# Kernel optimization log

Hardware: AMD Instinct MI355X
Metric: run time of the kernel (lower is better)

The kernel has to match this reference:

```python
import jax, jax.numpy as jnp
import numpy as np

B, S, D = 4, 4096, 1024
DC = 1024  # d_chunk (defaults to d_model)
NUM_CLASSES = 4


def setup_inputs() -> dict:
    key = jax.random.key(0)
    ks = jax.random.split(key, 8)
    init = lambda k, shape: (jax.random.normal(k, shape, jnp.float32) * 0.02)
    return {
        "h": jax.random.normal(ks[0], (B, S, D), jnp.float32),
        "pseudo_labels": jax.random.randint(ks[1], (B, S), 0, NUM_CLASSES, jnp.int32),
        "Wl": init(ks[2], (D, NUM_CLASSES)), "bl": jnp.zeros((NUM_CLASSES,), jnp.float32),
        "Wq": init(ks[3], (D, DC)), "bq": jnp.zeros((DC,), jnp.float32),
        "Wk": init(ks[4], (D, DC)), "bk": jnp.zeros((DC,), jnp.float32),
        "Wv": init(ks[5], (D, D)), "bv": jnp.zeros((D,), jnp.float32),
        "Wo": init(ks[6], (D, D)), "bo": jnp.zeros((D,), jnp.float32),
    }


def _chunk_starts(labels):
    """BIOS chunking: label 0=B starts a chunk extended by following 1=I's;
    labels 1 (orphan I), 2=O, 3=S are singleton chunks. Returns bool [B,S]
    marking chunk starts. Parallel replacement for the torch while-loop."""
    def step(ext, lab):  # ext[b]: previous token can be extended by an I
        cont = (lab == 1) & ext          # this token continues prev chunk
        new_ext = (lab == 0) | cont      # B, or a continuing I, is extendable
        return new_ext, ~cont            # non-continuing token starts a chunk
    init = jnp.zeros(labels.shape[0], dtype=bool)
    _, starts_t = jax.lax.scan(step, init, labels.T)  # scan over seq axis
    return starts_t.T  # [B, S]


def reference(h, pseudo_labels, Wl, bl, Wq, bq, Wk, bk, Wv, bv, Wo, bo):
    b, s, d = h.shape
    dc = Wq.shape[1]

    logits = h @ Wl + bl                                  # [B,S,4]
    logp = jax.nn.log_softmax(logits, axis=-1)
    loss = -jnp.mean(jnp.take_along_axis(logp, pseudo_labels[..., None], axis=-1))

    pred = jnp.argmax(logits, axis=-1).astype(jnp.int32)  # [B,S]
    starts = _chunk_starts(pred)
    seg = jnp.cumsum(starts.astype(jnp.int32), axis=1) - 1  # segment id per token

    # Segment-mean pooling, padded to S possible chunks per batch element.
    seg_sum = jax.vmap(lambda x, ids: jax.ops.segment_sum(x, ids, num_segments=s))(h, seg)
    counts = jax.vmap(lambda ids: jax.ops.segment_sum(jnp.ones((s,), h.dtype), ids, num_segments=s))(seg)
    chunk_emb = seg_sum / jnp.maximum(counts, 1.0)[..., None]  # [B,S,D]
    valid = counts > 0                                         # [B,S]

    q = h @ Wq + bq              # [B,S,DC]
    k = chunk_emb @ Wk + bk      # [B,C,DC]
    v = chunk_emb @ Wv + bv      # [B,C,D]
    scale = jnp.asarray(1.0 / np.sqrt(dc), h.dtype)
    scores = jnp.einsum('bsd,bcd->bsc', q, k) * scale
    scores = jnp.where(valid[:, None, :], scores, jnp.asarray(-1e30, h.dtype))
    attn = jax.nn.softmax(scores, axis=-1)
    attended = jnp.einsum('bsc,bcd->bsd', attn, v)
    ch_out = attended @ Wo + bo
    return ch_out, loss
```

## Files before the change

kernel.cpp:

```cpp
#include <hip/hip_runtime.h>

typedef unsigned short u16;
typedef __attribute__((ext_vector_type(8))) short short8;
typedef __attribute__((ext_vector_type(8))) unsigned short ushort8;
typedef __attribute__((ext_vector_type(4))) unsigned short ushort4v;
typedef __attribute__((ext_vector_type(4))) float f32x4;

#define NB 4
#define SS 4096
#define DD 1024
#define CFENCE asm volatile("" ::: "memory")

__device__ __forceinline__ u16 f2bf(float x) {
  unsigned u = __builtin_bit_cast(unsigned, x);
  u = (u + 0x7FFFu + ((u >> 16) & 1u)) >> 16;
  return (u16)u;
}
__device__ __forceinline__ float bf2f(u16 b) {
  unsigned u = ((unsigned)b) << 16;
  return __builtin_bit_cast(float, u);
}
__device__ __forceinline__ void gload16(const void* g, void* l) {
  __builtin_amdgcn_global_load_lds((const __attribute__((address_space(1))) void*)g,
                                   (__attribute__((address_space(3))) void*)l, 16, 0, 0);
}
__device__ __forceinline__ int xcd_swz(int bid, int nwg) {
  const int x = bid & 7, idx = bid >> 3;
  const int q = nwg >> 3, r = nwg & 7;
  return (x < r ? x * (q + 1) : r * (q + 1) + (x - r) * q) + idx;
}

__global__ __launch_bounds__(256) void k_logits(
    const float* __restrict__ h, const int* __restrict__ lab,
    const float* __restrict__ Wl, const float* __restrict__ bl,
    u16* __restrict__ h16, int* __restrict__ pred, float* __restrict__ lossPart)
{
  const int t = threadIdx.x, w = t >> 6, lane = t & 63;
  const int tok = blockIdx.x * 4 + w;
  const float4* h4p = (const float4*)(h + (size_t)tok * DD);
  const float4* wl4 = (const float4*)Wl;
  float p0 = 0.f, p1 = 0.f, p2 = 0.f, p3 = 0.f;
#pragma unroll
  for (int i = 0; i < 4; ++i) {
    const int d = i * 256 + lane * 4;
    float4 hv = h4p[i * 64 + lane];
    ushort4v hb;
    hb[0] = f2bf(hv.x); hb[1] = f2bf(hv.y); hb[2] = f2bf(hv.z); hb[3] = f2bf(hv.w);
    *(ushort4v*)(h16 + (size_t)tok * DD + d) = hb;
    float4 w0 = wl4[d], w1 = wl4[d + 1], w2 = wl4[d + 2], w3 = wl4[d + 3];
    p0 += hv.x * w0.x + hv.y * w1.x + hv.z * w2.x + hv.w * w3.x;
    p1 += hv.x * w0.y + hv.y * w1.y + hv.z * w2.y + hv.w * w3.y;
    p2 += hv.x * w0.z + hv.y * w1.z + hv.z * w2.z + hv.w * w3.z;
    p3 += hv.x * w0.w + hv.y * w1.w + hv.z * w2.w + hv.w * w3.w;
  }
#pragma unroll
  for (int m = 32; m; m >>= 1) {
    p0 += __shfl_xor(p0, m); p1 += __shfl_xor(p1, m);
    p2 += __shfl_xor(p2, m); p3 += __shfl_xor(p3, m);
  }
  __shared__ float ls[4];
  if (lane == 0) {
    float l[4] = {p0 + bl[0], p1 + bl[1], p2 + bl[2], p3 + bl[3]};
    int bi = 0; float bv = l[0];
#pragma unroll
    for (int c = 1; c < 4; ++c) if (l[c] > bv) { bv = l[c]; bi = c; }
    pred[tok] = bi;
    float se = 0.f;
#pragma unroll
    for (int c = 0; c < 4; ++c) se += expf(l[c] - bv);
    float lse = bv + logf(se);
    ls[w] = lse - l[lab[tok]];
  }
  __syncthreads();
  if (t == 0) lossPart[blockIdx.x] = ls[0] + ls[1] + ls[2] + ls[3];
}

__global__ __launch_bounds__(256) void k_wconv(
    const float* __restrict__ W0, const float* __restrict__ W1,
    const float* __restrict__ W2, const float* __restrict__ W3,
    u16* __restrict__ Wt)
{
  const int gid = blockIdx.x * 256 + threadIdx.x;
  const int mat = gid >> 20;
  const int rem = gid & ((1 << 20) - 1);
  const int n = rem >> 10, k = rem & 1023;
  const float* W = (mat == 0) ? W0 : (mat == 1) ? W1 : (mat == 2) ? W2 : W3;
  Wt[((size_t)mat << 20) + (size_t)n * 1024 + k] = f2bf(W[(size_t)k * 1024 + n]);
}

__global__ __launch_bounds__(256) void k_scan(
    const int* __restrict__ pred, int* __restrict__ cstart, int* __restrict__ ccnt)
{
  const int b = blockIdx.x, t = threadIdx.x;
  const int4* p4 = (const int4*)(pred + (size_t)b * SS);
  int labv[16];
#pragma unroll
  for (int i = 0; i < 4; ++i) {
    int4 v = p4[t * 4 + i];
    labv[i * 4 + 0] = v.x; labv[i * 4 + 1] = v.y;
    labv[i * 4 + 2] = v.z; labv[i * 4 + 3] = v.w;
  }
  int A = 0, Bc = 1;
#pragma unroll
  for (int e = 0; e < 16; ++e) {
    int a = (labv[e] == 0), bb = (labv[e] == 1);
    A = a | (bb & A);
    Bc = bb & Bc;
  }
  __shared__ int sA[256], sB[256], sC[256];
  sA[t] = A; sB[t] = Bc;
  __syncthreads();
  for (int off = 1; off < 256; off <<= 1) {
    int pa = 0, pb = 1;
    if (t >= off) { pa = sA[t - off]; pb = sB[t - off]; }
    __syncthreads();
    A = A | (Bc & pa); Bc = Bc & pb;
    sA[t] = A; sB[t] = Bc;
    __syncthreads();
  }
  const int extIn = (t == 0) ? 0 : sA[t - 1];
  int ext = extIn, nst = 0;
#pragma unroll
  for (int e = 0; e < 16; ++e) {
    int cont = (labv[e] == 1) & ext;
    nst += !cont;
    ext = (labv[e] == 0) | cont;
  }
  sC[t] = nst;
  __syncthreads();
  int tot = nst;
  for (int off = 1; off < 256; off <<= 1) {
    int pc = 0;
    if (t >= off) pc = sC[t - off];
    __syncthreads();
    tot += pc;
    sC[t] = tot;
    __syncthreads();
  }
  const int base = tot - nst;
  const int total = sC[255];
  if (t == 0) { ccnt[b] = total; cstart[b * (SS + 1) + total] = SS; }
  ext = extIn; int id = base;
#pragma unroll
  for (int e = 0; e < 16; ++e) {
    int cont = (labv[e] == 1) & ext;
    if (!cont) cstart[b * (SS + 1) + id++] = t * 16 + e;
    ext = (labv[e] == 0) | cont;
  }
}

__global__ __launch_bounds__(256) void k_pool(
    const float* __restrict__ h, const int* __restrict__ cstart,
    const int* __restrict__ ccnt, u16* __restrict__ cemb)
{
  const int t = threadIdx.x, w = t >> 6, lane = t & 63;
  const int gw = blockIdx.x * 4 + w;
  const int b = gw >> 12, c = gw & (SS - 1);
  u16* out = cemb + (size_t)gw * DD + lane * 16;
  if (c >= ccnt[b]) {
    ushort8 z = {0, 0, 0, 0, 0, 0, 0, 0};
    *(ushort8*)out = z; *(ushort8*)(out + 8) = z;
    return;
  }
  const int s0 = cstart[b * (SS + 1) + c], s1 = cstart[b * (SS + 1) + c + 1];
  float acc[16] = {};
  for (int s = s0; s < s1; ++s) {
    const float4* hp = (const float4*)(h + ((size_t)b * SS + s) * DD + lane * 16);
#pragma unroll
    for (int ii = 0; ii < 4; ++ii) {
      float4 v = hp[ii];
      acc[ii * 4 + 0] += v.x; acc[ii * 4 + 1] += v.y;
      acc[ii * 4 + 2] += v.z; acc[ii * 4 + 3] += v.w;
    }
  }
  const float inv = 1.f / (float)(s1 - s0);
  ushort8 o0, o1;
#pragma unroll
  for (int e = 0; e < 8; ++e) { o0[e] = f2bf(acc[e] * inv); o1[e] = f2bf(acc[8 + e] * inv); }
  *(ushort8*)out = o0; *(ushort8*)(out + 8) = o1;
}

template <int OUTF32>
__global__ __launch_bounds__(512, 2) void gemm256(
    const u16* __restrict__ A0, const u16* __restrict__ A1,
    const u16* __restrict__ A2, const u16* __restrict__ A3,
    const u16* __restrict__ Bt, long strideB,
    void* __restrict__ C0, void* __restrict__ C1,
    void* __restrict__ C2, void* __restrict__ C3,
    const float* __restrict__ bias, float scale, int M, int N, int K)
{
  __shared__ u16 lds[65536];
  u16* ldsA = lds;
  u16* ldsB = lds + 32768;
  const int t = threadIdx.x, lane = t & 63, w = t >> 6;
  const int wr = w >> 2, wc = w & 3;
  const int z = blockIdx.z;
  const u16* A = (z == 0) ? A0 : (z == 1) ? A1 : (z == 2) ? A2 : A3;
  void* Cp    = (z == 0) ? C0 : (z == 1) ? C1 : (z == 2) ? C2 : C3;
  const u16* B = Bt + (size_t)z * strideB;
  const int bid = blockIdx.y * gridDim.x + blockIdx.x;
  const int swz = xcd_swz(bid, gridDim.x * gridDim.y);
  const int m0 = (swz / gridDim.x) * 256, n0 = (swz % gridDim.x) * 256;

  f32x4 acc[8][4];
#pragma unroll
  for (int i = 0; i < 8; ++i)
#pragma unroll
    for (int j = 0; j < 4; ++j) acc[i][j] = (f32x4){0.f, 0.f, 0.f, 0.f};

  const int trow = t >> 3;
  const u16* Ag = A + (size_t)(m0 + trow) * K + ((t & 7) ^ (trow & 7)) * 8;
  const u16* Bg = B + (size_t)(n0 + trow) * K + ((t & 7) ^ (trow & 7)) * 8;
  u16* dA = ldsA + t * 8;
  u16* dB = ldsB + t * 8;

#define STG_A0(BUF, KT) { gload16(Ag + (size_t)(KT),            dA + (BUF) * 16384 + 0 * 4096); \
                          gload16(Ag + (size_t)128 * K + (KT),  dA + (BUF) * 16384 + 2 * 4096); }
#define STG_A1(BUF, KT) { gload16(Ag + (size_t)64 * K + (KT),   dA + (BUF) * 16384 + 1 * 4096); \
                          gload16(Ag + (size_t)192 * K + (KT),  dA + (BUF) * 16384 + 3 * 4096); }
#define STG_B0(BUF, KT) { gload16(Bg + (size_t)(KT),            dB + (BUF) * 16384 + 0 * 4096); \
                          gload16(Bg + (size_t)64 * K + (KT),   dB + (BUF) * 16384 + 1 * 4096); }
#define STG_B1(BUF, KT) { gload16(Bg + (size_t)128 * K + (KT),  dB + (BUF) * 16384 + 2 * 4096); \
                          gload16(Bg + (size_t)192 * K + (KT),  dB + (BUF) * 16384 + 3 * 4096); }
#define MFMA16(MH, NH, BF) \
  { _Pragma("unroll") for (int ks = 0; ks < 2; ++ks) \
    _Pragma("unroll") for (int mi = 0; mi < 4; ++mi) \
      _Pragma("unroll") for (int ni = 0; ni < 2; ++ni) \
        acc[(MH) * 4 + mi][(NH) * 2 + ni] = __builtin_amdgcn_mfma_f32_16x16x32_bf16( \
            af[mi][ks], BF[ni][ks], acc[(MH) * 4 + mi][(NH) * 2 + ni], 0, 0, 0); }

  const int lrow = lane & 15, hi = lane >> 4;
  const int co0 = (hi ^ (lrow & 7)) * 8;
  const int co1 = ((4 + hi) ^ (lrow & 7)) * 8;

  const int NT = K >> 6;
  STG_A0(0, 0); STG_B0(0, 0); STG_B1(0, 0); STG_A1(0, 0);
  if (NT > 1) { STG_A0(1, 64); STG_B0(1, 64); STG_B1(1, 64); }
  if (NT > 1) asm volatile("s_waitcnt vmcnt(6)" ::: "memory");
  else        asm volatile("s_waitcnt vmcnt(0)" ::: "memory");
  __builtin_amdgcn_s_barrier();
  CFENCE;

  for (int j = 0; j < NT; ++j) {
    const int cur = j & 1;
    const u16* bA = ldsA + cur * 16384;
    const u16* bB = ldsB + cur * 16384;
    const int kt1 = (j + 1) << 6, kt2 = (j + 2) << 6;
    short8 af[4][2], b0[2][2], b1[2][2];
#pragma unroll
    for (int mi = 0; mi < 4; ++mi) {
      af[mi][0] = *(const short8*)(bA + (wr * 128 + mi * 16 + lrow) * 64 + co0);
      af[mi][1] = *(const short8*)(bA + (wr * 128 + mi * 16 + lrow) * 64 + co1);
    }
#pragma unroll
    for (int ni = 0; ni < 2; ++ni) {
      b0[ni][0] = *(const short8*)(bB + (wc * 32 + ni * 16 + lrow) * 64 + co0);
      b0[ni][1] = *(const short8*)(bB + (wc * 32 + ni * 16 + lrow) * 64 + co1);
    }
    if (j + 1 < NT) STG_A1(cur ^ 1, kt1);
    CFENCE;
    __builtin_amdgcn_s_barrier();
    __builtin_amdgcn_s_setprio(1);
    MFMA16(0, 0, b0);
    __builtin_amdgcn_s_setprio(0);
    __builtin_amdgcn_sched_barrier(0);
    __builtin_amdgcn_s_barrier();
    CFENCE;
#pragma unroll
    for (int ni = 0; ni < 2; ++ni) {
      b1[ni][0] = *(const short8*)(bB + (128 + wc * 32 + ni * 16 + lrow) * 64 + co0);
      b1[ni][1] = *(const short8*)(bB + (128 + wc * 32 + ni * 16 + lrow) * 64 + co1);
    }
    if (j + 2 < NT) STG_A0(cur, kt2);
    CFENCE;
    __builtin_amdgcn_s_barrier();
    __builtin_amdgcn_s_setprio(1);
    MFMA16(0, 1, b1);
    __builtin_amdgcn_s_setprio(0);
    __builtin_amdgcn_sched_barrier(0);
    __builtin_amdgcn_s_barrier();
    CFENCE;
#pragma unroll
    for (int mi = 0; mi < 4; ++mi) {
      af[mi][0] = *(const short8*)(bA + (wr * 128 + 64 + mi * 16 + lrow) * 64 + co0);
      af[mi][1] = *(const short8*)(bA + (wr * 128 + 64 + mi * 16 + lrow) * 64 + co1);
    }
    if (j + 2 < NT) STG_B0(cur, kt2);
    CFENCE;
    __builtin_amdgcn_s_barrier();
    __builtin_amdgcn_s_setprio(1);
    MFMA16(1, 0, b0);
    __builtin_amdgcn_s_setprio(0);
    __builtin_amdgcn_sched_barrier(0);
    __builtin_amdgcn_s_barrier();
    CFENCE;
    if (j + 2 < NT) STG_B1(cur, kt2);
    CFENCE;
    __builtin_amdgcn_s_barrier();
    __builtin_amdgcn_s_setprio(1);
    MFMA16(1, 1, b1);
    __builtin_amdgcn_s_setprio(0);
    if (j < NT - 2)       asm volatile("s_waitcnt vmcnt(6)" ::: "memory");
    else if (j == NT - 2) asm volatile("s_waitcnt vmcnt(0)" ::: "memory");
    __builtin_amdgcn_sched_barrier(0);
    __builtin_amdgcn_s_barrier();
    CFENCE;
  }

  if (OUTF32) {
    const int rowb = m0 + wr * 128 + (lane >> 4) * 4;
#pragma unroll
    for (int n = 0; n < 4; ++n) {
      const int col = n0 + (n >> 1) * 128 + wc * 32 + (n & 1) * 16 + (lane & 15);
      const float bv = bias ? bias[col] : 0.f;
#pragma unroll
      for (int m = 0; m < 8; ++m)
#pragma unroll
        for (int q = 0; q < 4; ++q)
          ((float*)Cp)[(size_t)(rowb + m * 16 + q) * N + col] = acc[m][n][q] * scale + bv;
    }
  } else {
    u16* cls = lds;
    const int rowl = wr * 128 + (lane >> 4) * 4;
#pragma unroll
    for (int n = 0; n < 4; ++n) {
      const int coll = (n >> 1) * 128 + wc * 32 + (n & 1) * 16 + (lane & 15);
      const float bv = bias ? bias[n0 + coll] : 0.f;
#pragma unroll
      for (int m = 0; m < 8; ++m)
#pragma unroll
        for (int q = 0; q < 4; ++q)
          cls[(rowl + m * 16 + q) * 256 + coll] = f2bf(acc[m][n][q] * scale + bv);
    }
    __syncthreads();
    u16* Cu = (u16*)Cp;
#pragma unroll
    for (int ps = 0; ps < 16; ++ps) {
      const int f = ps * 512 + t;
      const int row = f >> 5, col8 = (f & 31) * 8;
      *(ushort8*)(Cu + (size_t)(m0 + row) * N + n0 + col8) =
          *(const ushort8*)(cls + row * 256 + col8);
    }
  }
#undef STG_A0
#undef STG_A1
#undef STG_B0
#undef STG_B1
#undef MFMA16
}

__global__ __launch_bounds__(256) void k_softmax(
    u16* __restrict__ s0, u16* __restrict__ s1,
    u16* __restrict__ s2, u16* __restrict__ s3, const int* __restrict__ ccnt)
{
  const int t = threadIdx.x, lane = t & 63, w = t >> 6;
  const int row = blockIdx.x, b = blockIdx.y;
  u16* sc = (b == 0) ? s0 : (b == 1) ? s1 : (b == 2) ? s2 : s3;
  const int Cb = ccnt[b];
  u16* p = sc + (size_t)row * SS + t * 16;
  ushort8 v0 = *(ushort8*)p, v1 = *(ushort8*)(p + 8);
  float x[16];
#pragma unroll
  for (int e = 0; e < 8; ++e) { x[e] = bf2f(v0[e]); x[8 + e] = bf2f(v1[e]); }
  const int cb0 = t * 16;
  float m = -1e30f;
#pragma unroll
  for (int e = 0; e < 16; ++e) if (cb0 + e < Cb) m = fmaxf(m, x[e]);
#pragma unroll
  for (int off = 32; off; off >>= 1) m = fmaxf(m, __shfl_xor(m, off));
  __shared__ float red[4], red2[4];
  if (lane == 0) red[w] = m;
  __syncthreads();
  m = fmaxf(fmaxf(red[0], red[1]), fmaxf(red[2], red[3]));
  float ssum = 0.f;
#pragma unroll
  for (int e = 0; e < 16; ++e) {
    float ev = (cb0 + e < Cb) ? __expf(x[e] - m) : 0.f;
    x[e] = ev; ssum += ev;
  }
#pragma unroll
  for (int off = 32; off; off >>= 1) ssum += __shfl_xor(ssum, off);
  if (lane == 0) red2[w] = ssum;
  __syncthreads();
  ssum = red2[0] + red2[1] + red2[2] + red2[3];
  const float inv = 1.f / ssum;
#pragma unroll
  for (int e = 0; e < 8; ++e) { v0[e] = f2bf(x[e] * inv); v1[e] = f2bf(x[8 + e] * inv); }
  *(ushort8*)p = v0; *(ushort8*)(p + 8) = v1;
}

__global__ __launch_bounds__(256) void k_transpose(
    const u16* __restrict__ v, u16* __restrict__ vt)
{
  __shared__ u16 ts[64][80];
  const int t = threadIdx.x;
  const int d0 = blockIdx.x * 64, c0 = blockIdx.y * 64, b = blockIdx.z;
#pragma unroll
  for (int p = 0; p < 2; ++p) {
    const int idx = p * 256 + t, r = idx >> 3, cc = idx & 7;
    ushort8 val = *(const ushort8*)(v + ((size_t)b * SS + c0 + r) * DD + d0 + cc * 8);
    *(ushort8*)&ts[r][cc * 8] = val;
  }
  __syncthreads();
#pragma unroll
  for (int p = 0; p < 2; ++p) {
    const int idx = p * 256 + t, r = idx >> 3, cc = idx & 7;
    ushort8 o;
#pragma unroll
    for (int e = 0; e < 8; ++e) o[e] = ts[cc * 8 + e][r];
    *(ushort8*)(vt + ((size_t)b * DD + d0 + r) * SS + c0 + cc * 8) = o;
  }
}

__global__ __launch_bounds__(256) void k_lossfin(
    const float* __restrict__ part, float* __restrict__ out)
{
  const int t = threadIdx.x, lane = t & 63, w = t >> 6;
  float s = 0.f;
  for (int i = t; i < 4096; i += 256) s += part[i];
#pragma unroll
  for (int off = 32; off; off >>= 1) s += __shfl_xor(s, off);
  __shared__ float r[4];
  if (lane == 0) r[w] = s;
  __syncthreads();
  if (t == 0) out[0] = (r[0] + r[1] + r[2] + r[3]) * (1.f / (NB * SS));
}

extern "C" void kernel_launch(void* const* d_in, const int* in_sizes, int n_in,
                              void* d_out, int out_size, void* d_ws, size_t ws_size,
                              hipStream_t stream) {
  const float* h  = (const float*)d_in[0];
  const int* plab = (const int*)d_in[1];
  const float* Wl = (const float*)d_in[2];
  const float* bl = (const float*)d_in[3];
  const float* Wq = (const float*)d_in[4];
  const float* bq = (const float*)d_in[5];
  const float* Wk = (const float*)d_in[6];
  const float* bk = (const float*)d_in[7];
  const float* Wv = (const float*)d_in[8];
  const float* bv = (const float*)d_in[9];
  const float* Wo = (const float*)d_in[10];
  const float* bo = (const float*)d_in[11];
  float* out = (float*)d_out;

  char* ws = (char*)d_ws;
  const size_t SZ = (size_t)NB * SS * DD * 2;
  const size_t SD = (size_t)SS * DD;
  u16* h16      = (u16*)(ws + 0 * SZ);
  u16* cemb     = (u16*)(ws + 1 * SZ);
  u16* q        = (u16*)(ws + 2 * SZ);
  u16* kk       = (u16*)(ws + 3 * SZ);
  u16* vv       = (u16*)(ws + 4 * SZ);
  u16* vt       = (u16*)(ws + 5 * SZ);
  u16* Wt       = (u16*)(ws + 6 * SZ);
  char* ws2     = ws + 6 * SZ + (size_t)4 * 1024 * 1024 * 2;
  int* pred     = (int*)ws2;
  int* cstart   = (int*)(ws2 + 65536);
  int* ccnt     = (int*)(ws2 + 65536 + 4 * (SS + 1) * 4);
  float* lossPart = (float*)(ws2 + 65536 + 4 * (SS + 1) * 4 + 64);
  u16* s0 = (u16*)d_out;
  u16* s1 = (u16*)d_out + (size_t)SS * SS;
  u16* s2 = h16;
  u16* s3 = cemb;
  u16* att = vv;

  k_logits<<<dim3(NB * SS / 4), 256, 0, stream>>>(h, plab, Wl, bl, h16, pred, lossPart);
  k_wconv<<<dim3(4 * 1024 * 1024 / 256), 256, 0, stream>>>(Wq, Wk, Wv, Wo, Wt);
  k_scan<<<dim3(NB), 256, 0, stream>>>(pred, cstart, ccnt);
  k_pool<<<dim3(NB * SS / 4), 256, 0, stream>>>(h, cstart, ccnt, cemb);

  gemm256<0><<<dim3(DD / 256, NB * SS / 256, 1), 512, 0, stream>>>(
      h16, h16, h16, h16, Wt, 0, q, q, q, q, bq, 1.f, NB * SS, DD, DD);
  gemm256<0><<<dim3(DD / 256, NB * SS / 256, 1), 512, 0, stream>>>(
      cemb, cemb, cemb, cemb, Wt + (1 << 20), 0, kk, kk, kk, kk, bk, 1.f, NB * SS, DD, DD);
  gemm256<0><<<dim3(DD / 256, NB * SS / 256, 1), 512, 0, stream>>>(
      cemb, cemb, cemb, cemb, Wt + 2 * (1 << 20), 0, vv, vv, vv, vv, bv, 1.f, NB * SS, DD, DD);
  k_transpose<<<dim3(DD / 64, SS / 64, NB), 256, 0, stream>>>(vv, vt);

  const float scl = 1.f / 32.f;
  gemm256<0><<<dim3(SS / 256, SS / 256, NB), 512, 0, stream>>>(
      q, q + SD, q + 2 * SD, q + 3 * SD, kk, (long)SD,
      s0, s1, s2, s3, nullptr, scl, SS, SS, DD);
  k_softmax<<<dim3(SS, NB), 256, 0, stream>>>(s0, s1, s2, s3, ccnt);
  gemm256<0><<<dim3(DD / 256, SS / 256, NB), 512, 0, stream>>>(
      s0, s1, s2, s3, vt, (long)SD,
      att, att + SD, att + 2 * SD, att + 3 * SD, nullptr, 1.f, SS, DD, SS);
  gemm256<1><<<dim3(DD / 256, NB * SS / 256, 1), 512, 0, stream>>>(
      att, att, att, att, Wt + 3 * (1 << 20), 0, out, out, out, out, bo, 1.f, NB * SS, DD, DD);
  k_lossfin<<<dim3(1), 256, 0, stream>>>(lossPart, out + (size_t)NB * SS * DD);
}
```

Baseline: 535.2 us.

## Software-pipeline LDS fragment reads across MFMA phases and swizzle epilogue staging

Restructures the GEMM main loop so LDS fragment reads for the next phase are issued before the current MFMA block, using lgkmcnt waits instead of barriers. The quadrant order is changed to reuse A and B fragments across phases, and the next tile's first fragments are prefetched at the end of each iteration. The number of barriers per k-step is reduced. It also XOR-swizzles the bf16 epilogue staging in LDS to avoid bank conflicts, and adds a sync before the epilogue reuses LDS. The cost is more live registers and more fragile wait-count ordering.

After: 614.2 us. 14.8% more time.

```diff
diff --git a/kernel.cpp b/kernel.cpp
--- a/kernel.cpp
+++ b/kernel.cpp
@@ -182,8 +182,8 @@
 
 template <int OUTF32>
 __global__ __launch_bounds__(512, 2) void gemm256(
-    const u16* __restrict__ A0, const u16* __restrict__ A1,
-    const u16* __restrict__ A2, const u16* __restrict__ A3,
+    const u16* __restrict__ A0p, const u16* __restrict__ A1p,
+    const u16* __restrict__ A2p, const u16* __restrict__ A3p,
     const u16* __restrict__ Bt, long strideB,
     void* __restrict__ C0, void* __restrict__ C1,
     void* __restrict__ C2, void* __restrict__ C3,
@@ -195,7 +195,7 @@
   const int t = threadIdx.x, lane = t & 63, w = t >> 6;
   const int wr = w >> 2, wc = w & 3;
   const int z = blockIdx.z;
-  const u16* A = (z == 0) ? A0 : (z == 1) ? A1 : (z == 2) ? A2 : A3;
+  const u16* A = (z == 0) ? A0p : (z == 1) ? A1p : (z == 2) ? A2p : A3p;
   void* Cp    = (z == 0) ? C0 : (z == 1) ? C1 : (z == 2) ? C2 : C3;
   const u16* B = Bt + (size_t)z * strideB;
   const int bid = blockIdx.y * gridDim.x + blockIdx.x;
@@ -222,12 +222,20 @@
                           gload16(Bg + (size_t)64 * K + (KT),   dB + (BUF) * 16384 + 1 * 4096); }
 #define STG_B1(BUF, KT) { gload16(Bg + (size_t)128 * K + (KT),  dB + (BUF) * 16384 + 2 * 4096); \
                           gload16(Bg + (size_t)192 * K + (KT),  dB + (BUF) * 16384 + 3 * 4096); }
-#define MFMA16(MH, NH, BF) \
+#define RD_A(DST, BASE, ROFF) \
+  { _Pragma("unroll") for (int mi = 0; mi < 4; ++mi) { \
+      DST[mi][0] = *(const short8*)((BASE) + (wr * 128 + (ROFF) + mi * 16 + lrow) * 64 + co0); \
+      DST[mi][1] = *(const short8*)((BASE) + (wr * 128 + (ROFF) + mi * 16 + lrow) * 64 + co1); } }
+#define RD_B(DST, BASE, ROFF) \
+  { _Pragma("unroll") for (int ni = 0; ni < 2; ++ni) { \
+      DST[ni][0] = *(const short8*)((BASE) + ((ROFF) + wc * 32 + ni * 16 + lrow) * 64 + co0); \
+      DST[ni][1] = *(const short8*)((BASE) + ((ROFF) + wc * 32 + ni * 16 + lrow) * 64 + co1); } }
+#define MFMA16(MH, AF, BF, NOFF) \
   { _Pragma("unroll") for (int ks = 0; ks < 2; ++ks) \
     _Pragma("unroll") for (int mi = 0; mi < 4; ++mi) \
       _Pragma("unroll") for (int ni = 0; ni < 2; ++ni) \
-        acc[(MH) * 4 + mi][(NH) * 2 + ni] = __builtin_amdgcn_mfma_f32_16x16x32_bf16( \
-            af[mi][ks], BF[ni][ks], acc[(MH) * 4 + mi][(NH) * 2 + ni], 0, 0, 0); }
+        acc[(MH) * 4 + mi][(NOFF) + ni] = __builtin_amdgcn_mfma_f32_16x16x32_bf16( \
+            AF[mi][ks], BF[ni][ks], acc[(MH) * 4 + mi][(NOFF) + ni], 0, 0, 0); }
 
   const int lrow = lane & 15, hi = lane >> 4;
   const int co0 = (hi ^ (lrow & 7)) * 8;
@@ -235,74 +243,73 @@
 
   const int NT = K >> 6;
   STG_A0(0, 0); STG_B0(0, 0); STG_B1(0, 0); STG_A1(0, 0);
-  if (NT > 1) { STG_A0(1, 64); STG_B0(1, 64); STG_B1(1, 64); }
-  if (NT > 1) asm volatile("s_waitcnt vmcnt(6)" ::: "memory");
-  else        asm volatile("s_waitcnt vmcnt(0)" ::: "memory");
+  if (NT > 1) {
+    STG_A0(1, 64); STG_B0(1, 64); STG_B1(1, 64); STG_A1(1, 64);
+    asm volatile("s_waitcnt vmcnt(8)" ::: "memory");
+  } else {
+    asm volatile("s_waitcnt vmcnt(0)" ::: "memory");
+  }
   __builtin_amdgcn_s_barrier();
   CFENCE;
+  short8 afA[4][2], afB[4][2], bA[2][2], bB[2][2];
+  RD_A(afA, ldsA, 0);
+  RD_B(bA, ldsB, 0);
+  CFENCE;
 
   for (int j = 0; j < NT; ++j) {
     const int cur = j & 1;
-    const u16* bA = ldsA + cur * 16384;
-    const u16* bB = ldsB + cur * 16384;
-    const int kt1 = (j + 1) << 6, kt2 = (j + 2) << 6;
-    short8 af[4][2], b0[2][2], b1[2][2];
-#pragma unroll
-    for (int mi = 0; mi < 4; ++mi) {
-      af[mi][0] = *(const short8*)(bA + (wr * 128 + mi * 16 + lrow) * 64 + co0);
-      af[mi][1] = *(const short8*)(bA + (wr * 128 + mi * 16 + lrow) * 64 + co1);
+    const u16* bufA = ldsA + cur * 16384;
+    const u16* bufB = ldsB + cur * 16384;
+    const u16* nbufA = ldsA + (cur ^ 1) * 16384;
+    const u16* nbufB = ldsB + (cur ^ 1) * 16384;
+    const int kt2 = (j + 2) << 6;
+    RD_B(bB, bufB, 128);
+    CFENCE;
+    asm volatile("s_waitcnt lgkmcnt(4)" ::: "memory");
+    __builtin_amdgcn_sched_barrier(0);
+    __builtin_amdgcn_s_setprio(1);
+    MFMA16(0, afA, bA, 0);
+    __builtin_amdgcn_s_setprio(0);
+    __builtin_amdgcn_sched_barrier(0);
+    __builtin_amdgcn_s_barrier();
+    CFENCE;
+    RD_A(afB, bufA, 64);
+    if (j + 2 < NT) { STG_A0(cur, kt2); STG_B0(cur, kt2); }
+    CFENCE;
+    asm volatile("s_waitcnt lgkmcnt(8)" ::: "memory");
+    __builtin_amdgcn_sched_barrier(0);
+    __builtin_amdgcn_s_setprio(1);
+    MFMA16(0, afA, bB, 2);
+    __builtin_amdgcn_s_setprio(0);
+    __builtin_amdgcn_sched_barrier(0);
+    __builtin_amdgcn_s_barrier();
+    CFENCE;
+    if (j + 2 < NT) STG_B1(cur, kt2);
+    CFENCE;
+    asm volatile("s_waitcnt lgkmcnt(0)" ::: "memory");
+    __builtin_amdgcn_sched_barrier(0);
+    __builtin_amdgcn_s_setprio(1);
+    MFMA16(1, afB, bB, 2);
+    __builtin_amdgcn_s_setprio(0);
+    if (j + 1 < NT) {
+      if (j + 2 < NT) asm volatile("s_waitcnt vmcnt(6)" ::: "memory");
+      else            asm volatile("s_waitcnt vmcnt(0)" ::: "memory");
     }
-#pragma unroll
-    for (int ni = 0; ni < 2; ++ni) {
-      b0[ni][0] = *(const short8*)(bB + (wc * 32 + ni * 16 + lrow) * 64 + co0);
-      b0[ni][1] = *(const short8*)(bB + (wc * 32 + ni * 16 + lrow) * 64 + co1);
+    __builtin_amdgcn_sched_barrier(0);
+    __builtin_amdgcn_s_barrier();
+    CFENCE;
+    if (j + 2 < NT) STG_A1(cur, kt2);
+    CFENCE;
+    __builtin_amdgcn_sched_barrier(0);
+    __builtin_amdgcn_s_setprio(1);
+    MFMA16(1, afB, bA, 0);
+    __builtin_amdgcn_s_setprio(0);
+    __builtin_amdgcn_sched_barrier(0);
+    if (j + 1 < NT) {
+      RD_A(afA, nbufA, 0);
+      RD_B(bA, nbufB, 0);
     }
-    if (j + 1 < NT) STG_A1(cur ^ 1, kt1);
-    CFENCE;
-    __builtin_amdgcn_s_barrier();
-    __builtin_amdgcn_s_setprio(1);
-    MFMA16(0, 0, b0);
-    __builtin_amdgcn_s_setprio(0);
-    __builtin_amdgcn_sched_barrier(0);
-    __builtin_amdgcn_s_barrier();
-    CFENCE;
-#pragma unroll
-    for (int ni = 0; ni < 2; ++ni) {
-      b1[ni][0] = *(const short8*)(bB + (128 + wc * 32 + ni * 16 + lrow) * 64 + co0);
-      b1[ni][1] = *(const short8*)(bB + (128 + wc * 32 + ni * 16 + lrow) * 64 + co1);
-    }
-    if (j + 2 < NT) STG_A0(cur, kt2);
-    CFENCE;
-    __builtin_amdgcn_s_barrier();
-    __builtin_amdgcn_s_setprio(1);
-    MFMA16(0, 1, b1);
-    __builtin_amdgcn_s_setprio(0);
-    __builtin_amdgcn_sched_barrier(0);
-    __builtin_amdgcn_s_barrier();
-    CFENCE;
-#pragma unroll
-    for (int mi = 0; mi < 4; ++mi) {
-      af[mi][0] = *(const short8*)(bA + (wr * 128 + 64 + mi * 16 + lrow) * 64 + co0);
-      af[mi][1] = *(const short8*)(bA + (wr * 128 + 64 + mi * 16 + lrow) * 64 + co1);
-    }
-    if (j + 2 < NT) STG_B0(cur, kt2);
-    CFENCE;
-    __builtin_amdgcn_s_barrier();
-    __builtin_amdgcn_s_setprio(1);
-    MFMA16(1, 0, b0);
-    __builtin_amdgcn_s_setprio(0);
-    __builtin_amdgcn_sched_barrier(0);
-    __builtin_amdgcn_s_barrier();
-    CFENCE;
-    if (j + 2 < NT) STG_B1(cur, kt2);
-    CFENCE;
-    __builtin_amdgcn_s_barrier();
-    __builtin_amdgcn_s_setprio(1);
-    MFMA16(1, 1, b1);
-    __builtin_amdgcn_s_setprio(0);
-    if (j < NT - 2)       asm volatile("s_waitcnt vmcnt(6)" ::: "memory");
-    else if (j == NT - 2) asm volatile("s_waitcnt vmcnt(0)" ::: "memory");
-    __builtin_amdgcn_sched_barrier(0);
+    CFENCE;
     __builtin_amdgcn_s_barrier();
     CFENCE;
   }
@@ -320,6 +327,7 @@
           ((float*)Cp)[(size_t)(rowb + m * 16 + q) * N + col] = acc[m][n][q] * scale + bv;
     }
   } else {
+    __syncthreads();
     u16* cls = lds;
     const int rowl = wr * 128 + (lane >> 4) * 4;
 #pragma unroll
@@ -329,23 +337,28 @@
 #pragma unroll
       for (int m = 0; m < 8; ++m)
 #pragma unroll
-        for (int q = 0; q < 4; ++q)
-          cls[(rowl + m * 16 + q) * 256 + coll] = f2bf(acc[m][n][q] * scale + bv);
+        for (int q = 0; q < 4; ++q) {
+          const int row = rowl + m * 16 + q;
+          cls[row * 256 + (coll ^ (((row >> 2) & 3) << 4))] = f2bf(acc[m][n][q] * scale + bv);
+        }
     }
     __syncthreads();
     u16* Cu = (u16*)Cp;
 #pragma unroll
     for (int ps = 0; ps < 16; ++ps) {
       const int f = ps * 512 + t;
-      const int row = f >> 5, col8 = (f & 31) * 8;
-      *(ushort8*)(Cu + (size_t)(m0 + row) * N + n0 + col8) =
-          *(const ushort8*)(cls + row * 256 + col8);
+      const int row = f >> 5, col8 = (f & 31);
+      const int scol8 = col8 ^ (((row >> 2) & 3) << 1);
+      *(ushort8*)(Cu + (size_t)(m0 + row) * N + n0 + col8 * 8) =
+          *(const ushort8*)(cls + row * 256 + scol8 * 8);
     }
   }
 #undef STG_A0
 #undef STG_A1
 #undef STG_B0
 #undef STG_B1
+#undef RD_A
+#undef RD_B
 #undef MFMA16
 }
 
```
